# Performance work log

Hardware: AMD Instinct MI355X
Metric: run time of the kernel (lower is better)

## Reference

```python
import jax, jax.numpy as jnp
import numpy as np

N = 20000      # atoms
E = 320000     # edges
F = 128        # node_size (hard-pinned by split(128) / expand to 384)
RBF = 20
RC = 5.0
ITERS = 3
NM = 64        # molecules in batch


def setup_inputs() -> dict:
    key = jax.random.key(0)
    ks = iter(jax.random.split(key, 64))
    def nrm(shape, scale=0.05):
        return jax.random.normal(next(ks), shape, dtype=jnp.float32) * scale
    inp = {}
    inp["z"] = jax.random.randint(next(ks), (N,), 0, 119)
    inp["graph"] = jax.random.randint(next(ks), (E, 2), 0, N)
    inp["edges_dist"] = jax.random.uniform(next(ks), (E,), minval=0.5, maxval=RC, dtype=jnp.float32)
    sense = jax.random.normal(next(ks), (E, 3), dtype=jnp.float32)
    inp["edges_sense"] = sense / jnp.linalg.norm(sense, axis=1, keepdims=True)
    inp["graph_idx"] = jnp.sort(jax.random.randint(next(ks), (N,), 0, NM))
    # parameters (stacked over ITERS message/update blocks)
    inp["emb"] = nrm((119, F), 1.0)
    inp["mw1"] = nrm((ITERS, F, F)); inp["mb1"] = nrm((ITERS, F))
    inp["mw2"] = nrm((ITERS, 3 * F, F)); inp["mb2"] = nrm((ITERS, 3 * F))
    inp["ew"] = nrm((ITERS, 3 * F, RBF)); inp["eb"] = nrm((ITERS, 3 * F))
    inp["uw"] = nrm((ITERS, F, F)); inp["vw"] = nrm((ITERS, F, F))
    inp["aw1"] = nrm((ITERS, F, 2 * F)); inp["ab1"] = nrm((ITERS, F))
    inp["aw2"] = nrm((ITERS, 3 * F, F)); inp["ab2"] = nrm((ITERS, 3 * F))
    inp["ow1"] = nrm((F, F)); inp["ob1"] = nrm((F,))
    inp["ow2"] = nrm((1, F)); inp["ob2"] = nrm((1,))
    return inp


def reference(z, graph, edges_dist, edges_sense, graph_idx,
              emb, mw1, mb1, mw2, mb2, ew, eb,
              uw, vw, aw1, ab1, aw2, ab2, ow1, ob1, ow2, ob2):
    src = graph[:, 0]   # scatter target (index_add index)
    dst = graph[:, 1]   # gather source (neighbour)
    s = emb[z]                                  # [N, F]
    v = jnp.zeros((N, 3, F), dtype=s.dtype)     # [N, 3, F]
    # edge-level precompute (same every iteration)
    n = jnp.arange(1, RBF + 1, dtype=jnp.float32)
    d = edges_dist[:, None]
    rbf = jnp.sin(n * jnp.pi * d / RC) / d                              # [E, RBF]
    cut = 0.5 * (jnp.cos(jnp.pi * edges_dist / RC) + 1.0) * (edges_dist < RC)  # [E]
    for i in range(ITERS):
        # --- Message block ---
        a = jax.nn.silu(s @ mw1[i].T + mb1[i]) @ mw2[i].T + mb2[i]      # [N, 3F]
        dist_rep = (rbf @ ew[i].T + eb[i]) * cut[:, None]               # [E, 3F]
        res = a[dst] * dist_rep                                         # [E, 3F]
        rv, rs, rd = res[:, :F], res[:, F:2 * F], res[:, 2 * F:]
        resv = v[dst] * rv[:, None, :] + edges_sense[:, :, None] * rd[:, None, :]  # [E,3,F]
        s = s + 2.0 * jax.ops.segment_sum(rs, src, num_segments=N)
        v = v + 2.0 * jax.ops.segment_sum(resv, src, num_segments=N)
        # --- Update block ---
        Uv = v @ uw[i].T                                                # [N,3,F]
        Vv = v @ vw[i].T
        h = jnp.concatenate([s, jnp.linalg.norm(Vv, axis=1)], axis=-1)  # [N, 2F]
        a2 = jax.nn.silu(h @ aw1[i].T + ab1[i]) @ aw2[i].T + ab2[i]     # [N, 3F]
        avv, asv, ass = a2[:, :F], a2[:, F:2 * F], a2[:, 2 * F:]
        s = s + ass + asv * jnp.sum(Uv * Vv, axis=1)
        v = v + avv[:, None, :] * Uv
    out = jax.nn.silu(s @ ow1.T + ob1) @ ow2.T + ob2                    # [N, 1]
    return jax.ops.segment_sum(out, graph_idx, num_segments=NM)         # [NM, 1]
```

## Files before the change

kernel.cpp:

```cpp
#include <hip/hip_runtime.h>
#include <math.h>

#define NN 20000
#define NE 320000
#define FD 128
#define RBFN 20
#define RC_ 5.0f
#define NITER 3
#define NMOL 64
#define F3 384
#define F2 256
#define PI_ 3.14159265358979323846f
#define KB 128
#define LPAD 8
#define SDS 392

typedef __attribute__((ext_vector_type(8))) short  bf16x8;
typedef __attribute__((ext_vector_type(4))) float  floatx4;
typedef unsigned short u16;
typedef unsigned int   u32;

__device__ __forceinline__ u16 f2b(float x) {
    union { float f; unsigned int u; } v; v.f = x;
    unsigned int u = v.u;
    return (u16)((u + 0x7fffu + ((u >> 16) & 1u)) >> 16);
}
__device__ __forceinline__ float b2f(u16 x) {
    union { unsigned int u; float f; } v; v.u = ((unsigned int)x) << 16;
    return v.f;
}
__device__ __forceinline__ float blo(u32 w) {
    union { unsigned int u; float f; } v; v.u = w << 16; return v.f;
}
__device__ __forceinline__ float bhi(u32 w) {
    union { unsigned int u; float f; } v; v.u = w & 0xffff0000u; return v.f;
}
__device__ __forceinline__ u32 pack2(float a, float b) {
    return (u32)f2b(a) | ((u32)f2b(b) << 16);
}

__global__ __launch_bounds__(256) void init_all_kernel(
    const float* s0, int n0, const float* s1, int n1, const float* s2, int n2,
    const float* s3, int n3, const float* s4, int n4, const float* s5, int n5,
    const float* s6, int n6, u16* __restrict__ wdst,
    const float* __restrict__ ew, u16* __restrict__ ewb,
    const int* __restrict__ z, const float* __restrict__ emb,
    float* __restrict__ s, u16* __restrict__ sbf,
    float* __restrict__ v_a, int* __restrict__ v_pk_i, int* __restrict__ cnt)
{
    int idx = blockIdx.x * 256 + threadIdx.x;
    if (idx < NN * F3) v_a[idx] = 0.f;
    if (idx < NN * F3 / 2) v_pk_i[idx] = 0;
    if (idx < NN) cnt[idx] = 0;
    if (idx < NN * FD) {
        int n = idx >> 7, f = idx & 127;
        float v = emb[z[n] * FD + f];
        s[idx] = v; sbf[idx] = f2b(v);
    }
    if (idx < NITER * F3 * 32) {
        int k = idx & 31;
        int row = idx >> 5;
        ewb[idx] = (k < RBFN) ? f2b(ew[row * RBFN + k]) : (u16)0;
    }
    {
        int w = idx;
        u16* dst = wdst;
        if (w < n0) { dst[w] = f2b(s0[w]); return; } w -= n0; dst += n0;
        if (w < n1) { dst[w] = f2b(s1[w]); return; } w -= n1; dst += n1;
        if (w < n2) { dst[w] = f2b(s2[w]); return; } w -= n2; dst += n2;
        if (w < n3) { dst[w] = f2b(s3[w]); return; } w -= n3; dst += n3;
        if (w < n4) { dst[w] = f2b(s4[w]); return; } w -= n4; dst += n4;
        if (w < n5) { dst[w] = f2b(s5[w]); return; } w -= n5; dst += n5;
        if (w < n6) { dst[w] = f2b(s6[w]); }
    }
}

__global__ __launch_bounds__(256) void csr_count_kernel(const int* __restrict__ graph,
    int* __restrict__ cnt)
{
    int e = blockIdx.x * 256 + threadIdx.x;
    if (e >= NE) return;
    atomicAdd(&cnt[graph[2 * e]], 1);
}

__global__ __launch_bounds__(1024) void csr_scan_kernel(const int* __restrict__ cnt,
    int* __restrict__ row_ptr, int* __restrict__ cursor)
{
    __shared__ int sd[1024];
    int tid = threadIdx.x;
    const int chunk = (NN + 1023) / 1024;
    int start = tid * chunk;
    int end = start + chunk; if (end > NN) end = NN;
    int sum = 0;
    for (int j = start; j < end; j++) sum += cnt[j];
    sd[tid] = sum;
    __syncthreads();
    for (int off = 1; off < 1024; off <<= 1) {
        int v = 0;
        if (tid >= off) v = sd[tid - off];
        __syncthreads();
        if (tid >= off) sd[tid] += v;
        __syncthreads();
    }
    int run = (tid == 0) ? 0 : sd[tid - 1];
    for (int j = start; j < end; j++) {
        row_ptr[j] = run;
        cursor[j]  = run;
        run += cnt[j];
    }
    if (tid == 0) row_ptr[NN] = NE;
}

__global__ __launch_bounds__(256) void csr_scatter_kernel(const int* __restrict__ graph,
    int* __restrict__ cursor, int* __restrict__ edge_list)
{
    int e = blockIdx.x * 256 + threadIdx.x;
    if (e >= NE) return;
    int p = atomicAdd(&cursor[graph[2 * e]], 1);
    edge_list[p] = e;
}

__global__ __launch_bounds__(256) void edge_stream_kernel(
    const int* __restrict__ edge_list, const int* __restrict__ graph,
    const float* __restrict__ dist, const float* __restrict__ sense,
    u16* __restrict__ rbf_bf, float* __restrict__ cut_p,
    float* __restrict__ sense_p, int* __restrict__ dst_p)
{
    int j = blockIdx.x * 256 + threadIdx.x;
    if (j >= NE) return;
    int e = edge_list[j];
    float d = dist[e];
    float inv = 1.f / d;
    float base = PI_ * d / RC_;
    float s1, c1;
    __sincosf(base, &s1, &c1);
    float twoc = c1 + c1;
    u16* rb = rbf_bf + (size_t)j * 32;
    float sprev = 0.f, scur = s1;
    #pragma unroll
    for (int k = 0; k < RBFN; k++) {
        rb[k] = f2b(scur * inv);
        float snext = twoc * scur - sprev;
        sprev = scur; scur = snext;
    }
    #pragma unroll
    for (int k = RBFN; k < 32; k++) rb[k] = 0;
    cut_p[j] = 0.5f * (c1 + 1.f) * (d < RC_ ? 1.f : 0.f);
    dst_p[j] = graph[2 * e + 1];
    sense_p[3 * j + 0] = sense[3 * e + 0];
    sense_p[3 * j + 1] = sense[3 * e + 1];
    sense_p[3 * j + 2] = sense[3 * e + 2];
}

template<int K1, bool PACK>
__global__ __launch_bounds__(256) void mlp_kernel(const u16* __restrict__ A,
    const u16* __restrict__ W1, const float* __restrict__ b1,
    const u16* __restrict__ W2, const float* __restrict__ b2,
    u16* __restrict__ Ob, int M)
{
    __shared__ u16 As[64][KB + LPAD];
    __shared__ u16 Ws[128][KB + LPAD];
    __shared__ u16 T[64][KB + LPAD];
    const int bm = blockIdx.x * 64;
    const int tid = threadIdx.x;
    const int wave = tid >> 6, lane = tid & 63;
    const int wm  = (wave >> 1) * 32;
    const int wn1 = (wave & 1) * 64;
    const int wn  = (wave & 1) * 32;
    const int quad = lane >> 4, lr = lane & 15;
    const int r = tid >> 2, q = tid & 3;

    floatx4 acc1[2][4];
    #pragma unroll
    for (int i = 0; i < 2; i++)
        #pragma unroll
        for (int j = 0; j < 4; j++) acc1[i][j] = (floatx4)0.f;

    for (int ko = 0; ko < K1; ko += KB) {
        {
            int gm = bm + r;
            u16* dA = &As[r][q * 32];
            if (gm < M) {
                const u16* ap = A + (size_t)gm * K1 + ko + q * 32;
                #pragma unroll
                for (int x = 0; x < 32; x += 8)
                    *(bf16x8*)&dA[x] = *(const bf16x8*)(ap + x);
            } else {
                #pragma unroll
                for (int x = 0; x < 32; x += 8)
                    *(bf16x8*)&dA[x] = (bf16x8)0;
            }
            #pragma unroll
            for (int h = 0; h < 2; h++) {
                int wr = r + h * 64;
                const u16* wp = W1 + (size_t)wr * K1 + ko + q * 32;
                u16* dW = &Ws[wr][q * 32];
                #pragma unroll
                for (int x = 0; x < 32; x += 8)
                    *(bf16x8*)&dW[x] = *(const bf16x8*)(wp + x);
            }
        }
        __syncthreads();
        #pragma unroll
        for (int kk = 0; kk < KB; kk += 32) {
            bf16x8 a0 = *(const bf16x8*)&As[wm + lr     ][kk + quad * 8];
            bf16x8 a1 = *(const bf16x8*)&As[wm + 16 + lr][kk + quad * 8];
            #pragma unroll
            for (int j = 0; j < 4; j++) {
                bf16x8 b = *(const bf16x8*)&Ws[wn1 + j * 16 + lr][kk + quad * 8];
                acc1[0][j] = __builtin_amdgcn_mfma_f32_16x16x32_bf16(a0, b, acc1[0][j], 0, 0, 0);
                acc1[1][j] = __builtin_amdgcn_mfma_f32_16x16x32_bf16(a1, b, acc1[1][j], 0, 0, 0);
            }
        }
        __syncthreads();
    }
    #pragma unroll
    for (int i = 0; i < 2; i++) {
        #pragma unroll
        for (int j = 0; j < 4; j++) {
            int col = wn1 + j * 16 + lr;
            float bb = b1[col];
            #pragma unroll
            for (int rr = 0; rr < 4; rr++) {
                int row = wm + i * 16 + quad * 4 + rr;
                float v = acc1[i][j][rr] + bb;
                v = v / (1.f + __expf(-v));
                T[row][col] = f2b(v);
            }
        }
    }
    __syncthreads();

    for (int c0 = 0; c0 < F3; c0 += 64) {
        {
            const u16* wp = W2 + (size_t)(c0 + r) * KB + q * 32;
            u16* dW = &Ws[r][q * 32];
            #pragma unroll
            for (int x = 0; x < 32; x += 8)
                *(bf16x8*)&dW[x] = *(const bf16x8*)(wp + x);
        }
        __syncthreads();
        floatx4 acc2[2][2];
        #pragma unroll
        for (int i = 0; i < 2; i++)
            #pragma unroll
            for (int j = 0; j < 2; j++) acc2[i][j] = (floatx4)0.f;
        #pragma unroll
        for (int kk = 0; kk < KB; kk += 32) {
            bf16x8 a0 = *(const bf16x8*)&T[wm + lr     ][kk + quad * 8];
            bf16x8 a1 = *(const bf16x8*)&T[wm + 16 + lr][kk + quad * 8];
            bf16x8 b0 = *(const bf16x8*)&Ws[wn + lr     ][kk + quad * 8];
            bf16x8 b1 = *(const bf16x8*)&Ws[wn + 16 + lr][kk + quad * 8];
            acc2[0][0] = __builtin_amdgcn_mfma_f32_16x16x32_bf16(a0, b0, acc2[0][0], 0, 0, 0);
            acc2[0][1] = __builtin_amdgcn_mfma_f32_16x16x32_bf16(a0, b1, acc2[0][1], 0, 0, 0);
            acc2[1][0] = __builtin_amdgcn_mfma_f32_16x16x32_bf16(a1, b0, acc2[1][0], 0, 0, 0);
            acc2[1][1] = __builtin_amdgcn_mfma_f32_16x16x32_bf16(a1, b1, acc2[1][1], 0, 0, 0);
        }
        #pragma unroll
        for (int i = 0; i < 2; i++) {
            #pragma unroll
            for (int j = 0; j < 2; j++) {
                int gn = c0 + wn + j * 16 + lr;
                float bb = b2[gn];
                #pragma unroll
                for (int rr = 0; rr < 4; rr++) {
                    int gm = bm + wm + i * 16 + quad * 4 + rr;
                    if (gm < M) {
                        u16 val = f2b(acc2[i][j][rr] + bb);
                        if (PACK) {
                            int off = (gn < 256) ? ((gn & 127) * 2 + (gn >> 7))
                                                 : (256 + (gn & 127));
                            Ob[(size_t)gm * F3 + off] = val;
                        } else {
                            Ob[(size_t)gm * F3 + gn] = val;
                        }
                    }
                }
            }
        }
        __syncthreads();
    }
}

__global__ __launch_bounds__(256) void gemm_uv(const u16* __restrict__ A,
    const u16* __restrict__ Wu, const u16* __restrict__ Wv,
    u16* __restrict__ U, u16* __restrict__ V, int M)
{
    __shared__ u16 As[64][KB + LPAD];
    __shared__ u16 Bu[64][KB + LPAD];
    __shared__ u16 Bv[64][KB + LPAD];
    const int bm = blockIdx.x * 64;
    const int bn = blockIdx.y * 64;
    const int tid = threadIdx.x;
    const int r = tid >> 2;
    const int q = tid & 3;
    const int wave = tid >> 6;
    const int lane = tid & 63;
    const int wm = (wave >> 1) * 32;
    const int wn = (wave & 1) * 32;
    const int quad = lane >> 4;
    const int lr = lane & 15;

    floatx4 au[2][2], av[2][2];
    #pragma unroll
    for (int i = 0; i < 2; i++)
        #pragma unroll
        for (int j = 0; j < 2; j++) { au[i][j] = (floatx4)0.f; av[i][j] = (floatx4)0.f; }

    {
        int gm = bm + r;
        u16* dA = &As[r][q * 32];
        if (gm < M) {
            const u16* ap = A + (size_t)gm * KB + q * 32;
            #pragma unroll
            for (int x = 0; x < 32; x += 8)
                *(bf16x8*)&dA[x] = *(const bf16x8*)(ap + x);
        } else {
            #pragma unroll
            for (int x = 0; x < 32; x += 8)
                *(bf16x8*)&dA[x] = (bf16x8)0;
        }
        int gn = bn + r;
        const u16* up = Wu + (size_t)gn * KB + q * 32;
        const u16* vp = Wv + (size_t)gn * KB + q * 32;
        u16* dU = &Bu[r][q * 32];
        u16* dV = &Bv[r][q * 32];
        #pragma unroll
        for (int x = 0; x < 32; x += 8) {
            *(bf16x8*)&dU[x] = *(const bf16x8*)(up + x);
            *(bf16x8*)&dV[x] = *(const bf16x8*)(vp + x);
        }
    }
    __syncthreads();
    #pragma unroll
    for (int kk = 0; kk < KB; kk += 32) {
        bf16x8 a0 = *(const bf16x8*)&As[wm + lr     ][kk + quad * 8];
        bf16x8 a1 = *(const bf16x8*)&As[wm + 16 + lr][kk + quad * 8];
        bf16x8 u0 = *(const bf16x8*)&Bu[wn + lr     ][kk + quad * 8];
        bf16x8 u1 = *(const bf16x8*)&Bu[wn + 16 + lr][kk + quad * 8];
        bf16x8 v0 = *(const bf16x8*)&Bv[wn + lr     ][kk + quad * 8];
        bf16x8 v1 = *(const bf16x8*)&Bv[wn + 16 + lr][kk + quad * 8];
        au[0][0] = __builtin_amdgcn_mfma_f32_16x16x32_bf16(a0, u0, au[0][0], 0, 0, 0);
        au[0][1] = __builtin_amdgcn_mfma_f32_16x16x32_bf16(a0, u1, au[0][1], 0, 0, 0);
        au[1][0] = __builtin_amdgcn_mfma_f32_16x16x32_bf16(a1, u0, au[1][0], 0, 0, 0);
        au[1][1] = __builtin_amdgcn_mfma_f32_16x16x32_bf16(a1, u1, au[1][1], 0, 0, 0);
        av[0][0] = __builtin_amdgcn_mfma_f32_16x16x32_bf16(a0, v0, av[0][0], 0, 0, 0);
        av[0][1] = __builtin_amdgcn_mfma_f32_16x16x32_bf16(a0, v1, av[0][1], 0, 0, 0);
        av[1][0] = __builtin_amdgcn_mfma_f32_16x16x32_bf16(a1, v0, av[1][0], 0, 0, 0);
        av[1][1] = __builtin_amdgcn_mfma_f32_16x16x32_bf16(a1, v1, av[1][1], 0, 0, 0);
    }
    #pragma unroll
    for (int i = 0; i < 2; i++) {
        #pragma unroll
        for (int j = 0; j < 2; j++) {
            int gn = bn + wn + j * 16 + lr;
            #pragma unroll
            for (int rr = 0; rr < 4; rr++) {
                int gm = bm + wm + i * 16 + quad * 4 + rr;
                if (gm < M) {
                    U[(size_t)gm * FD + gn] = f2b(au[i][j][rr]);
                    V[(size_t)gm * FD + gn] = f2b(av[i][j][rr]);
                }
            }
        }
    }
}

__global__ __launch_bounds__(256) void edge_mfma_kernel(
    const u16* __restrict__ rbf_bf, const float* __restrict__ cut_p,
    const float* __restrict__ sense_p, const int* __restrict__ dst_p,
    const u16* __restrict__ ewb, const float* __restrict__ eb,
    const u16* __restrict__ a_pk, const float* __restrict__ s_in,
    const float* __restrict__ v_in, const u16* __restrict__ v_pk,
    const int* __restrict__ row_ptr,
    float* __restrict__ s_out, u16* __restrict__ s_obf,
    float* __restrict__ v_out, u16* __restrict__ v_obf)
{
    __shared__ u16   sdrep[16 * SDS];
    __shared__ float scut[16];
    __shared__ float ssen[16][4];
    __shared__ int   sdst[16];
    __shared__ float red[4 * 128];

    const int n = blockIdx.x;
    const int tid = threadIdx.x;
    const int wave = tid >> 6;
    const int lane = tid & 63;
    const int quad = lane >> 4;
    const int lr = lane & 15;
    const int f = tid & 127;
    const int half = tid >> 7;

    int beg = row_ptr[n], end = row_ptr[n + 1];
    float accs = 0.f, accv0 = 0.f, accv1 = 0.f, accv2 = 0.f;

    for (int t0 = beg; t0 < end; t0 += 16) {
        int cnt = end - t0; if (cnt > 16) cnt = 16;
        __syncthreads();
        if (tid < 16) {
            scut[tid] = (tid < cnt) ? cut_p[t0 + tid] : 0.f;
            sdst[tid] = (tid < cnt) ? dst_p[t0 + tid] : 0;
        }
        if (tid >= 64 && tid < 64 + 3 * cnt) {
            int x = tid - 64;
            ssen[x / 3][x % 3] = sense_p[3 * t0 + x];
        }
        bf16x8 afrag;
        int ge = t0 + lr;
        if (ge < end) afrag = *(const bf16x8*)&rbf_bf[(size_t)ge * 32 + quad * 8];
        else          afrag = (bf16x8)0;
        floatx4 dacc[6];
        #pragma unroll
        for (int nt = 0; nt < 6; nt++) {
            int nrow = (wave * 6 + nt) * 16 + lr;
            bf16x8 bfrag = *(const bf16x8*)&ewb[(size_t)nrow * 32 + quad * 8];
            dacc[nt] = __builtin_amdgcn_mfma_f32_16x16x32_bf16(afrag, bfrag, (floatx4)0.f, 0, 0, 0);
        }
        __syncthreads();
        #pragma unroll
        for (int nt = 0; nt < 6; nt++) {
            int ncol = (wave * 6 + nt) * 16 + lr;
            float ebn = eb[ncol];
            #pragma unroll
            for (int rr = 0; rr < 4; rr++) {
                int e = quad * 4 + rr;
                sdrep[e * SDS + ncol] = f2b((dacc[nt][rr] + ebn) * scut[e]);
            }
        }
        __syncthreads();
        int nh = cnt - half * 8; if (nh > 8) nh = 8;
        for (int k = 0; k < nh; k++) {
            int e = half * 8 + k;
            int dst = sdst[e];
            const u16* sr = &sdrep[e * SDS];
            float drv = b2f(sr[f]);
            float drs = b2f(sr[FD + f]);
            float drd = b2f(sr[2 * FD + f]);
            const u16* ar = a_pk + (size_t)dst * F3;
            u32 ap = *(const u32*)(ar + f * 2);
            float rv = b2f((u16)(ap & 0xffff)) * drv;
            float rs = b2f((u16)(ap >> 16))    * drs;
            float rd = b2f(ar[256 + f])        * drd;
            accs += rs;
            const u16* vr = v_pk + (size_t)dst * F3;
            u32 vp = *(const u32*)(vr + f * 2);
            accv0 += b2f((u16)(vp & 0xffff)) * rv + ssen[e][0] * rd;
            accv1 += b2f((u16)(vp >> 16))    * rv + ssen[e][1] * rd;
            accv2 += b2f(vr[256 + f])        * rv + ssen[e][2] * rd;
        }
    }
    __syncthreads();
    if (half == 1) {
        red[f] = accs; red[128 + f] = accv0; red[256 + f] = accv1; red[384 + f] = accv2;
    }
    __syncthreads();
    if (half == 0) {
        accs  += red[f];       accv0 += red[128 + f];
        accv1 += red[256 + f]; accv2 += red[384 + f];
        int nb = n * FD + f;
        float so = s_in[nb] + 2.f * accs;
        s_out[nb] = so; s_obf[nb] = f2b(so);
        int vb = n * F3 + f;
        float w0 = v_in[vb]           + 2.f * accv0;
        float w1 = v_in[vb + FD]      + 2.f * accv1;
        float w2 = v_in[vb + 2 * FD]  + 2.f * accv2;
        v_out[vb]          = w0; v_obf[vb]          = f2b(w0);
        v_out[vb + FD]     = w1; v_obf[vb + FD]     = f2b(w1);
        v_out[vb + 2 * FD] = w2; v_obf[vb + 2 * FD] = f2b(w2);
    }
}

template<bool LAST>
__global__ __launch_bounds__(256) void mlp2_update_next_kernel(
    const u16* __restrict__ sbf_mid, const float* __restrict__ s_mid,
    const float* __restrict__ v_mid,
    const u16* __restrict__ Uv, const u16* __restrict__ Vv,
    const u16* __restrict__ W1, const float* __restrict__ b1,
    const u16* __restrict__ W2, const float* __restrict__ b2,
    float* __restrict__ s_out,
    float* __restrict__ v_out, u16* __restrict__ v_pk,
    const u16* __restrict__ N_W1, const float* __restrict__ N_b1,
    const u16* __restrict__ N_W2, const float* __restrict__ N_b2,
    u16* __restrict__ a_pk,
    const u16* __restrict__ H_W1, const float* __restrict__ H_b1,
    const float* __restrict__ ow2, const float* __restrict__ ob2,
    float* __restrict__ nodeval, int M)
{
    __shared__ u16 As[64][KB + LPAD];
    __shared__ u16 Ws[128][KB + LPAD];
    __shared__ u16 T[64][KB + LPAD];
    const int bm = blockIdx.x * 64;
    const int tid = threadIdx.x;
    const int wave = tid >> 6, lane = tid & 63;
    const int wm  = (wave >> 1) * 32;
    const int wn1 = (wave & 1) * 64;
    const int wn  = (wave & 1) * 32;
    const int quad = lane >> 4, lr = lane & 15;
    const int r = tid >> 2, q = tid & 3;

    floatx4 acc1[2][4];
    #pragma unroll
    for (int i = 0; i < 2; i++)
        #pragma unroll
        for (int j = 0; j < 4; j++) acc1[i][j] = (floatx4)0.f;

    {
        int gm = bm + r;
        u16* dA = &As[r][q * 32];
        if (gm < M) {
            const u16* ap = sbf_mid + (size_t)gm * FD + q * 32;
            #pragma unroll
            for (int x = 0; x < 32; x += 8)
                *(bf16x8*)&dA[x] = *(const bf16x8*)(ap + x);
        } else {
            #pragma unroll
            for (int x = 0; x < 32; x += 8)
                *(bf16x8*)&dA[x] = (bf16x8)0;
        }
        #pragma unroll
        for (int h = 0; h < 2; h++) {
            int wr = r + h * 64;
            const u16* wp = W1 + (size_t)wr * F2 + q * 32;
            u16* dW = &Ws[wr][q * 32];
            #pragma unroll
            for (int x = 0; x < 32; x += 8)
                *(bf16x8*)&dW[x] = *(const bf16x8*)(wp + x);
        }
    }
    __syncthreads();
    #pragma unroll
    for (int kk = 0; kk < KB; kk += 32) {
        bf16x8 a0 = *(const bf16x8*)&As[wm + lr     ][kk + quad * 8];
        bf16x8 a1 = *(const bf16x8*)&As[wm + 16 + lr][kk + quad * 8];
        #pragma unroll
        for (int j = 0; j < 4; j++) {
            bf16x8 b = *(const bf16x8*)&Ws[wn1 + j * 16 + lr][kk + quad * 8];
            acc1[0][j] = __builtin_amdgcn_mfma_f32_16x16x32_bf16(a0, b, acc1[0][j], 0, 0, 0);
            acc1[1][j] = __builtin_amdgcn_mfma_f32_16x16x32_bf16(a1, b, acc1[1][j], 0, 0, 0);
        }
    }
    __syncthreads();
    {
        int gm = bm + r;
        u16* dA = &As[r][q * 32];
        if (gm < M) {
            const u16* vvp = Vv + (size_t)gm * F3 + q * 32;
            bf16x8 c0[4], c1[4], c2[4];
            #pragma unroll
            for (int t = 0; t < 4; t++) {
                c0[t] = *(const bf16x8*)(vvp + t * 8);
                c1[t] = *(const bf16x8*)(vvp + FD + t * 8);
                c2[t] = *(const bf16x8*)(vvp + 2 * FD + t * 8);
            }
            #pragma unroll
            for (int t = 0; t < 4; t++) {
                #pragma unroll
                for (int x = 0; x < 8; x++) {
                    float a = b2f((u16)c0[t][x]);
                    float b = b2f((u16)c1[t][x]);
                    float c = b2f((u16)c2[t][x]);
                    dA[t * 8 + x] = f2b(sqrtf(a * a + b * b + c * c));
                }
            }
        } else {
            #pragma unroll
            for (int x = 0; x < 32; x += 8)
                *(bf16x8*)&dA[x] = (bf16x8)0;
        }
        #pragma unroll
        for (int h = 0; h < 2; h++) {
            int wr = r + h * 64;
            const u16* wp = W1 + (size_t)wr * F2 + KB + q * 32;
            u16* dW = &Ws[wr][q * 32];
            #pragma unroll
            for (int x = 0; x < 32; x += 8)
                *(bf16x8*)&dW[x] = *(const bf16x8*)(wp + x);
        }
    }
    __syncthreads();
    #pragma unroll
    for (int kk = 0; kk < KB; kk += 32) {
        bf16x8 a0 = *(const bf16x8*)&As[wm + lr     ][kk + quad * 8];
        bf16x8 a1 = *(const bf16x8*)&As[wm + 16 + lr][kk + quad * 8];
        #pragma unroll
        for (int j = 0; j < 4; j++) {
            bf16x8 b = *(const bf16x8*)&Ws[wn1 + j * 16 + lr][kk + quad * 8];
            acc1[0][j] = __builtin_amdgcn_mfma_f32_16x16x32_bf16(a0, b, acc1[0][j], 0, 0, 0);
            acc1[1][j] = __builtin_amdgcn_mfma_f32_16x16x32_bf16(a1, b, acc1[1][j], 0, 0, 0);
        }
    }
    __syncthreads();
    #pragma unroll
    for (int i = 0; i < 2; i++) {
        #pragma unroll
        for (int j = 0; j < 4; j++) {
            int col = wn1 + j * 16 + lr;
            float bb = b1[col];
            #pragma unroll
            for (int rr = 0; rr < 4; rr++) {
                int row = wm + i * 16 + quad * 4 + rr;
                float v = acc1[i][j][rr] + bb;
                v = v / (1.f + __expf(-v));
                T[row][col] = f2b(v);
            }
        }
    }
    __syncthreads();

    float avvr[2][2][4], asvr[2][2][4];
    #pragma unroll
    for (int part = 0; part < 2; part++) {
        #pragma unroll
        for (int piece = 0; piece < 3; piece++) {
            const int c0 = piece * 128 + part * 64;
            {
                const u16* wp = W2 + (size_t)(c0 + r) * KB + q * 32;
                u16* dW = &Ws[r][q * 32];
                #pragma unroll
                for (int x = 0; x < 32; x += 8)
                    *(bf16x8*)&dW[x] = *(const bf16x8*)(wp + x);
            }
            __syncthreads();
            floatx4 acc2[2][2];
            #pragma unroll
            for (int i = 0; i < 2; i++)
                #pragma unroll
                for (int j = 0; j < 2; j++) acc2[i][j] = (floatx4)0.f;
            #pragma unroll
            for (int kk = 0; kk < KB; kk += 32) {
                bf16x8 a0 = *(const bf16x8*)&T[wm + lr     ][kk + quad * 8];
                bf16x8 a1 = *(const bf16x8*)&T[wm + 16 + lr][kk + quad * 8];
                bf16x8 b0 = *(const bf16x8*)&Ws[wn + lr     ][kk + quad * 8];
                bf16x8 b1 = *(const bf16x8*)&Ws[wn + 16 + lr][kk + quad * 8];
                acc2[0][0] = __builtin_amdgcn_mfma_f32_16x16x32_bf16(a0, b0, acc2[0][0], 0, 0, 0);
                acc2[0][1] = __builtin_amdgcn_mfma_f32_16x16x32_bf16(a0, b1, acc2[0][1], 0, 0, 0);
                acc2[1][0] = __builtin_amdgcn_mfma_f32_16x16x32_bf16(a1, b0, acc2[1][0], 0, 0, 0);
                acc2[1][1] = __builtin_amdgcn_mfma_f32_16x16x32_bf16(a1, b1, acc2[1][1], 0, 0, 0);
            }
            if (piece == 0) {
                #pragma unroll
                for (int i = 0; i < 2; i++)
                    #pragma unroll
                    for (int j = 0; j < 2; j++) {
                        int gn = c0 + wn + j * 16 + lr;
                        float bb = b2[gn];
                        #pragma unroll
                        for (int rr = 0; rr < 4; rr++)
                            avvr[i][j][rr] = acc2[i][j][rr] + bb;
                    }
            } else if (piece == 1) {
                #pragma unroll
                for (int i = 0; i < 2; i++)
                    #pragma unroll
                    for (int j = 0; j < 2; j++) {
                        int gn = c0 + wn + j * 16 + lr;
                        float bb = b2[gn];
                        #pragma unroll
                        for (int rr = 0; rr < 4; rr++)
                            asvr[i][j][rr] = acc2[i][j][rr] + bb;
                    }
            } else {
                #pragma unroll
                for (int i = 0; i < 2; i++) {
                    #pragma unroll
                    for (int j = 0; j < 2; j++) {
                        int gn = c0 + wn + j * 16 + lr;
                        int f  = gn - 256;
                        float bb = b2[gn];
                        #pragma unroll
                        for (int rr = 0; rr < 4; rr++) {
                            int row = wm + i * 16 + quad * 4 + rr;
                            int gm = bm + row;
                            if (gm < M) {
                                float ass = acc2[i][j][rr] + bb;
                                float asv = asvr[i][j][rr];
                                float avv = avvr[i][j][rr];
                                int vb = gm * F3 + f;
                                float u0 = b2f(Uv[vb]);
                                float u1 = b2f(Uv[vb + FD]);
                                float u2 = b2f(Uv[vb + 2 * FD]);
                                float w0 = b2f(Vv[vb]);
                                float w1 = b2f(Vv[vb + FD]);
                                float w2 = b2f(Vv[vb + 2 * FD]);
                                float dot = u0 * w0 + u1 * w1 + u2 * w2;
                                int nb = gm * FD + f;
                                float so = s_mid[nb] + ass + asv * dot;
                                s_out[nb] = so;
                                As[row][f] = f2b(so);
                                float y0 = v_mid[vb]          + avv * u0;
                                float y1 = v_mid[vb + FD]     + avv * u1;
                                float y2 = v_mid[vb + 2 * FD] + avv * u2;
                                v_out[vb]          = y0;
                                v_out[vb + FD]     = y1;
                                v_out[vb + 2 * FD] = y2;
                                char* vpb = (char*)v_pk + (size_t)gm * (2 * F3);
                                *(u32*)(vpb + 4 * f) = pack2(y0, y1);
                                *(u16*)(vpb + 512 + 2 * f) = f2b(y2);
                            } else {
                                As[row][f] = 0;
                            }
                        }
                    }
                }
            }
            __syncthreads();
        }
    }

    if constexpr (!LAST) {
        {
            #pragma unroll
            for (int h = 0; h < 2; h++) {
                int wr = r + h * 64;
                const u16* wp = N_W1 + (size_t)wr * KB + q * 32;
                u16* dW = &Ws[wr][q * 32];
                #pragma unroll
                for (int x = 0; x < 32; x += 8)
                    *(bf16x8*)&dW[x] = *(const bf16x8*)(wp + x);
            }
        }
        __syncthreads();
        #pragma unroll
        for (int i = 0; i < 2; i++)
            #pragma unroll
            for (int j = 0; j < 4; j++) acc1[i][j] = (floatx4)0.f;
        #pragma unroll
        for (int kk = 0; kk < KB; kk += 32) {
            bf16x8 a0 = *(const bf16x8*)&As[wm + lr     ][kk + quad * 8];
            bf16x8 a1 = *(const bf16x8*)&As[wm + 16 + lr][kk + quad * 8];
            #pragma unroll
            for (int j = 0; j < 4; j++) {
                bf16x8 b = *(const bf16x8*)&Ws[wn1 + j * 16 + lr][kk + quad * 8];
                acc1[0][j] = __builtin_amdgcn_mfma_f32_16x16x32_bf16(a0, b, acc1[0][j], 0, 0, 0);
                acc1[1][j] = __builtin_amdgcn_mfma_f32_16x16x32_bf16(a1, b, acc1[1][j], 0, 0, 0);
            }
        }
        __syncthreads();
        #pragma unroll
        for (int i = 0; i < 2; i++) {
            #pragma unroll
            for (int j = 0; j < 4; j++) {
                int col = wn1 + j * 16 + lr;
                float bb = N_b1[col];
                #pragma unroll
                for (int rr = 0; rr < 4; rr++) {
                    int row = wm + i * 16 + quad * 4 + rr;
                    float v = acc1[i][j][rr] + bb;
                    v = v / (1.f + __expf(-v));
                    T[row][col] = f2b(v);
                }
            }
        }
        __syncthreads();
        for (int c0 = 0; c0 < F3; c0 += 64) {
            {
                const u16* wp = N_W2 + (size_t)(c0 + r) * KB + q * 32;
                u16* dW = &Ws[r][q * 32];
                #pragma unroll
                for (int x = 0; x < 32; x += 8)
                    *(bf16x8*)&dW[x] = *(const bf16x8*)(wp + x);
            }
            __syncthreads();
            floatx4 acc2[2][2];
            #pragma unroll
            for (int i = 0; i < 2; i++)
                #pragma unroll
                for (int j = 0; j < 2; j++) acc2[i][j] = (floatx4)0.f;
            #pragma unroll
            for (int kk = 0; kk < KB; kk += 32) {
                bf16x8 a0 = *(const bf16x8*)&T[wm + lr     ][kk + quad * 8];
                bf16x8 a1 = *(const bf16x8*)&T[wm + 16 + lr][kk + quad * 8];
                bf16x8 b0 = *(const bf16x8*)&Ws[wn + lr     ][kk + quad * 8];
                bf16x8 b1 = *(const bf16x8*)&Ws[wn + 16 + lr][kk + quad * 8];
                acc2[0][0] = __builtin_amdgcn_mfma_f32_16x16x32_bf16(a0, b0, acc2[0][0], 0, 0, 0);
                acc2[0][1] = __builtin_amdgcn_mfma_f32_16x16x32_bf16(a0, b1, acc2[0][1], 0, 0, 0);
                acc2[1][0] = __builtin_amdgcn_mfma_f32_16x16x32_bf16(a1, b0, acc2[1][0], 0, 0, 0);
                acc2[1][1] = __builtin_amdgcn_mfma_f32_16x16x32_bf16(a1, b1, acc2[1][1], 0, 0, 0);
            }
            #pragma unroll
            for (int i = 0; i < 2; i++) {
                #pragma unroll
                for (int j = 0; j < 2; j++) {
                    int gn = c0 + wn + j * 16 + lr;
                    float bb = N_b2[gn];
                    #pragma unroll
                    for (int rr = 0; rr < 4; rr++) {
                        int gm = bm + wm + i * 16 + quad * 4 + rr;
                        if (gm < M) {
                            u16 val = f2b(acc2[i][j][rr] + bb);
                            int off = (gn < 256) ? ((gn & 127) * 2 + (gn >> 7))
                                                 : (256 + (gn & 127));
                            a_pk[(size_t)gm * F3 + off] = val;
                        }
                    }
                }
            }
            __syncthreads();
        }
    } else {
        {
            #pragma unroll
            for (int h = 0; h < 2; h++) {
                int wr = r + h * 64;
                const u16* wp = H_W1 + (size_t)wr * KB + q * 32;
                u16* dW = &Ws[wr][q * 32];
                #pragma unroll
                for (int x = 0; x < 32; x += 8)
                    *(bf16x8*)&dW[x] = *(const bf16x8*)(wp + x);
            }
        }
        __syncthreads();
        #pragma unroll
        for (int i = 0; i < 2; i++)
            #pragma unroll
            for (int j = 0; j < 4; j++) acc1[i][j] = (floatx4)0.f;
        #pragma unroll
        for (int kk = 0; kk < KB; kk += 32) {
            bf16x8 a0 = *(const bf16x8*)&As[wm + lr     ][kk + quad * 8];
            bf16x8 a1 = *(const bf16x8*)&As[wm + 16 + lr][kk + quad * 8];
            #pragma unroll
            for (int j = 0; j < 4; j++) {
                bf16x8 b = *(const bf16x8*)&Ws[wn1 + j * 16 + lr][kk + quad * 8];
                acc1[0][j] = __builtin_amdgcn_mfma_f32_16x16x32_bf16(a0, b, acc1[0][j], 0, 0, 0);
                acc1[1][j] = __builtin_amdgcn_mfma_f32_16x16x32_bf16(a1, b, acc1[1][j], 0, 0, 0);
            }
        }
        __syncthreads();
        float* Tf   = (float*)&Ws[0][0];
        float* ow2s = (float*)&As[0][0];
        if (tid < KB) ow2s[tid] = ow2[tid];
        #pragma unroll
        for (int i = 0; i < 2; i++) {
            #pragma unroll
            for (int j = 0; j < 4; j++) {
                int col = wn1 + j * 16 + lr;
                float bb = H_b1[col];
                #pragma unroll
                for (int rr = 0; rr < 4; rr++) {
                    int row = wm + i * 16 + quad * 4 + rr;
                    float v = acc1[i][j][rr] + bb;
                    v = v / (1.f + __expf(-v));
                    Tf[row * 132 + col] = v;
                }
            }
        }
        __syncthreads();
        int nl = tid >> 2, seg = tid & 3;
        float v = 0.f;
        #pragma unroll
        for (int x = 0; x < 32; x++) {
            int col = seg * 32 + x;
            v += Tf[nl * 132 + col] * ow2s[col];
        }
        v += __shfl_down(v, 2);
        v += __shfl_down(v, 1);
        if (seg == 0) {
            int gm = bm + nl;
            if (gm < M) nodeval[gm] = v + ob2[0];
        }
    }
}

__global__ __launch_bounds__(1024) void mol_reduce_kernel(const float* __restrict__ nodeval,
    const int* __restrict__ gidx, float* __restrict__ out)
{
    __shared__ float mol[NMOL];
    int tid = threadIdx.x;
    if (tid < NMOL) mol[tid] = 0.f;
    __syncthreads();
    int cur = -1; float acc = 0.f;
    for (int x = tid; x < NN; x += 1024) {
        int g = gidx[x];
        float v = nodeval[x];
        if (g != cur) {
            if (cur >= 0) atomicAdd(&mol[cur], acc);
            cur = g; acc = v;
        } else acc += v;
    }
    if (cur >= 0) atomicAdd(&mol[cur], acc);
    __syncthreads();
    if (tid < NMOL) out[tid] = mol[tid];
}

extern "C" void kernel_launch(void* const* d_in, const int* in_sizes, int n_in,
                              void* d_out, int out_size, void* d_ws, size_t ws_size,
                              hipStream_t stream)
{
    const int*   z     = (const int*)d_in[0];
    const int*   graph = (const int*)d_in[1];
    const float* dist  = (const float*)d_in[2];
    const float* sense = (const float*)d_in[3];
    const int*   gidx  = (const int*)d_in[4];
    const float* emb   = (const float*)d_in[5];
    const float* mw1   = (const float*)d_in[6];
    const float* mb1   = (const float*)d_in[7];
    const float* mw2   = (const float*)d_in[8];
    const float* mb2   = (const float*)d_in[9];
    const float* ew    = (const float*)d_in[10];
    const float* eb    = (const float*)d_in[11];
    const float* uw    = (const float*)d_in[12];
    const float* vw    = (const float*)d_in[13];
    const float* aw1   = (const float*)d_in[14];
    const float* ab1   = (const float*)d_in[15];
    const float* aw2   = (const float*)d_in[16];
    const float* ab2   = (const float*)d_in[17];
    const float* ow1   = (const float*)d_in[18];
    const float* ob1   = (const float*)d_in[19];
    const float* ow2   = (const float*)d_in[20];
    const float* ob2   = (const float*)d_in[21];
    float* out = (float*)d_out;

    float* W = (float*)d_ws;
    float* s_a    = W; W += (size_t)NN * FD;
    float* s_b    = W; W += (size_t)NN * FD;
    float* v_a    = W; W += (size_t)NN * F3;
    float* v_b    = W; W += (size_t)NN * F3;
    float* cut_p  = W; W += (size_t)NE;
    float* sns_p  = W; W += (size_t)NE * 3;
    float* nodeval= W; W += (size_t)NN;
    u16* U = (u16*)W;
    u16* sbf_a = U; U += (size_t)NN * FD;
    u16* sbf_b = U; U += (size_t)NN * FD;
    u16* vbf_b = U; U += (size_t)NN * F3;
    u16* a_pk  = U; U += (size_t)NN * F3;
    u16* v_pk  = U; U += (size_t)NN * F3;
    u16* h_bf  = U; U += (size_t)NN * F2;
    u16* a2_bf = U; U += (size_t)NN * F3;
    u16* Uv_bf = U; U += (size_t)NN * F3;
    u16* Vv_bf = U; U += (size_t)NN * F3;
    u16* rbf_bf= U; U += (size_t)NE * 32;
    u16* ewb   = U; U += (size_t)NITER * F3 * 32;
    u16* wb    = U; U += 557056;
    int* ip = (int*)U;
    int* row_ptr   = ip; ip += NN + 1;
    int* cnt       = ip; ip += NN;
    int* cursor    = ip; ip += NN;
    int* edge_list = ip; ip += NE;
    int* dst_p     = ip; ip += NE;

    u16* wb_mw1 = wb;
    u16* wb_mw2 = wb + 49152;
    u16* wb_uw  = wb + 196608;
    u16* wb_vw  = wb + 245760;
    u16* wb_aw1 = wb + 294912;
    u16* wb_aw2 = wb + 393216;
    u16* wb_ow1 = wb + 540672;

    const int TB = 256;
    dim3 b256(TB);

    init_all_kernel<<<dim3((NN * F3 + TB - 1) / TB), b256, 0, stream>>>(
        mw1, 49152, mw2, 147456, uw, 49152, vw, 49152, aw1, 98304, aw2, 147456,
        ow1, 16384, wb, ew, ewb, z, emb, s_a, sbf_a, v_a, (int*)v_pk, cnt);
    csr_count_kernel<<<dim3((NE + TB - 1) / TB), b256, 0, stream>>>(graph, cnt);
    csr_scan_kernel<<<dim3(1), dim3(1024), 0, stream>>>(cnt, row_ptr, cursor);
    csr_scatter_kernel<<<dim3((NE + TB - 1) / TB), b256, 0, stream>>>(graph, cursor, edge_list);
    edge_stream_kernel<<<dim3((NE + TB - 1) / TB), b256, 0, stream>>>(
        edge_list, graph, dist, sense, rbf_bf, cut_p, sns_p, dst_p);

    dim3 gM((NN + 63) / 64);
    dim3 gV2((3 * NN + 63) / 64, FD / 64);

    mlp_kernel<128, true><<<gM, b256, 0, stream>>>(sbf_a,
        wb_mw1, mb1, wb_mw2, mb2, a_pk, NN);

    for (int i = 0; i < NITER; i++) {
        edge_mfma_kernel<<<dim3(NN), b256, 0, stream>>>(
            rbf_bf, cut_p, sns_p, dst_p,
            ewb + (size_t)i * F3 * 32, eb + (size_t)i * F3,
            a_pk, s_a, v_a, v_pk, row_ptr, s_b, sbf_b, v_b, vbf_b);
        gemm_uv<<<gV2, b256, 0, stream>>>(vbf_b, wb_uw + (size_t)i * FD * FD,
            wb_vw + (size_t)i * FD * FD, Uv_bf, Vv_bf, 3 * NN);
        if (i < NITER - 1) {
            mlp2_update_next_kernel<false><<<gM, b256, 0, stream>>>(
                sbf_b, s_b, v_b, Uv_bf, Vv_bf,
                wb_aw1 + (size_t)i * FD * F2, ab1 + (size_t)i * FD,
                wb_aw2 + (size_t)i * F3 * FD, ab2 + (size_t)i * F3,
                s_a, v_a, v_pk,
                wb_mw1 + (size_t)(i + 1) * FD * FD, mb1 + (size_t)(i + 1) * FD,
                wb_mw2 + (size_t)(i + 1) * F3 * FD, mb2 + (size_t)(i + 1) * F3, a_pk,
                nullptr, nullptr, nullptr, nullptr, nullptr, NN);
        } else {
            mlp2_update_next_kernel<true><<<gM, b256, 0, stream>>>(
                sbf_b, s_b, v_b, Uv_bf, Vv_bf,
                wb_aw1 + (size_t)i * FD * F2, ab1 + (size_t)i * FD,
                wb_aw2 + (size_t)i * F3 * FD, ab2 + (size_t)i * F3,
                s_a, v_a, v_pk,
                nullptr, nullptr, nullptr, nullptr, nullptr,
                wb_ow1, ob1, ow2, ob2, nodeval, NN);
        }
    }

    mol_reduce_kernel<<<dim3(1), dim3(1024), 0, stream>>>(nodeval, gidx, out);
}
```

Before: 868.5 us.

## Double-buffer W2 tiles in update MLP and merge gemm_uv column tiles

In the update/next-message kernel, the second-layer weight tiles are now double-buffered across two halves of the shared Ws buffer. Each 64-column slice is prefetched while the current one is multiplied, which removes one barrier per slice. gemm_uv now runs one block per 64-row tile and loops over both 64-column output tiles, so the A tile is loaded from global memory once instead of twice, at the cost of half as many blocks. This assumes Ws already has room for 128 rows; the diff does not change its declaration.

```diff
diff --git a/kernel.cpp b/kernel.cpp
--- a/kernel.cpp
+++ b/kernel.cpp
@@ -290,7 +290,6 @@
     __shared__ u16 Bu[64][KB + LPAD];
     __shared__ u16 Bv[64][KB + LPAD];
     const int bm = blockIdx.x * 64;
-    const int bn = blockIdx.y * 64;
     const int tid = threadIdx.x;
     const int r = tid >> 2;
     const int q = tid & 3;
@@ -301,12 +300,6 @@
     const int quad = lane >> 4;
     const int lr = lane & 15;
 
-    floatx4 au[2][2], av[2][2];
-    #pragma unroll
-    for (int i = 0; i < 2; i++)
-        #pragma unroll
-        for (int j = 0; j < 2; j++) { au[i][j] = (floatx4)0.f; av[i][j] = (floatx4)0.f; }
-
     {
         int gm = bm + r;
         u16* dA = &As[r][q * 32];
@@ -320,49 +313,61 @@
             for (int x = 0; x < 32; x += 8)
                 *(bf16x8*)&dA[x] = (bf16x8)0;
         }
-        int gn = bn + r;
-        const u16* up = Wu + (size_t)gn * KB + q * 32;
-        const u16* vp = Wv + (size_t)gn * KB + q * 32;
-        u16* dU = &Bu[r][q * 32];
-        u16* dV = &Bv[r][q * 32];
-        #pragma unroll
-        for (int x = 0; x < 32; x += 8) {
-            *(bf16x8*)&dU[x] = *(const bf16x8*)(up + x);
-            *(bf16x8*)&dV[x] = *(const bf16x8*)(vp + x);
-        }
-    }
-    __syncthreads();
+    }
+
     #pragma unroll
-    for (int kk = 0; kk < KB; kk += 32) {
-        bf16x8 a0 = *(const bf16x8*)&As[wm + lr     ][kk + quad * 8];
-        bf16x8 a1 = *(const bf16x8*)&As[wm + 16 + lr][kk + quad * 8];
-        bf16x8 u0 = *(const bf16x8*)&Bu[wn + lr     ][kk + quad * 8];
-        bf16x8 u1 = *(const bf16x8*)&Bu[wn + 16 + lr][kk + quad * 8];
-        bf16x8 v0 = *(const bf16x8*)&Bv[wn + lr     ][kk + quad * 8];
-        bf16x8 v1 = *(const bf16x8*)&Bv[wn + 16 + lr][kk + quad * 8];
-        au[0][0] = __builtin_amdgcn_mfma_f32_16x16x32_bf16(a0, u0, au[0][0], 0, 0, 0);
-        au[0][1] = __builtin_amdgcn_mfma_f32_16x16x32_bf16(a0, u1, au[0][1], 0, 0, 0);
-        au[1][0] = __builtin_amdgcn_mfma_f32_16x16x32_bf16(a1, u0, au[1][0], 0, 0, 0);
-        au[1][1] = __builtin_amdgcn_mfma_f32_16x16x32_bf16(a1, u1, au[1][1], 0, 0, 0);
-        av[0][0] = __builtin_amdgcn_mfma_f32_16x16x32_bf16(a0, v0, av[0][0], 0, 0, 0);
-        av[0][1] = __builtin_amdgcn_mfma_f32_16x16x32_bf16(a0, v1, av[0][1], 0, 0, 0);
-        av[1][0] = __builtin_amdgcn_mfma_f32_16x16x32_bf16(a1, v0, av[1][0], 0, 0, 0);
-        av[1][1] = __builtin_amdgcn_mfma_f32_16x16x32_bf16(a1, v1, av[1][1], 0, 0, 0);
-    }
-    #pragma unroll
-    for (int i = 0; i < 2; i++) {
-        #pragma unroll
-        for (int j = 0; j < 2; j++) {
-            int gn = bn + wn + j * 16 + lr;
-            #pragma unroll
-            for (int rr = 0; rr < 4; rr++) {
-                int gm = bm + wm + i * 16 + quad * 4 + rr;
-                if (gm < M) {
-                    U[(size_t)gm * FD + gn] = f2b(au[i][j][rr]);
-                    V[(size_t)gm * FD + gn] = f2b(av[i][j][rr]);
+    for (int bn = 0; bn < FD; bn += 64) {
+        {
+            int gn = bn + r;
+            const u16* up = Wu + (size_t)gn * KB + q * 32;
+            const u16* vp = Wv + (size_t)gn * KB + q * 32;
+            u16* dU = &Bu[r][q * 32];
+            u16* dV = &Bv[r][q * 32];
+            #pragma unroll
+            for (int x = 0; x < 32; x += 8) {
+                *(bf16x8*)&dU[x] = *(const bf16x8*)(up + x);
+                *(bf16x8*)&dV[x] = *(const bf16x8*)(vp + x);
+            }
+        }
+        __syncthreads();
+        floatx4 au[2][2], av[2][2];
+        #pragma unroll
+        for (int i = 0; i < 2; i++)
+            #pragma unroll
+            for (int j = 0; j < 2; j++) { au[i][j] = (floatx4)0.f; av[i][j] = (floatx4)0.f; }
+        #pragma unroll
+        for (int kk = 0; kk < KB; kk += 32) {
+            bf16x8 a0 = *(const bf16x8*)&As[wm + lr     ][kk + quad * 8];
+            bf16x8 a1 = *(const bf16x8*)&As[wm + 16 + lr][kk + quad * 8];
+            bf16x8 u0 = *(const bf16x8*)&Bu[wn + lr     ][kk + quad * 8];
+            bf16x8 u1 = *(const bf16x8*)&Bu[wn + 16 + lr][kk + quad * 8];
+            bf16x8 v0 = *(const bf16x8*)&Bv[wn + lr     ][kk + quad * 8];
+            bf16x8 v1 = *(const bf16x8*)&Bv[wn + 16 + lr][kk + quad * 8];
+            au[0][0] = __builtin_amdgcn_mfma_f32_16x16x32_bf16(a0, u0, au[0][0], 0, 0, 0);
+            au[0][1] = __builtin_amdgcn_mfma_f32_16x16x32_bf16(a0, u1, au[0][1], 0, 0, 0);
+            au[1][0] = __builtin_amdgcn_mfma_f32_16x16x32_bf16(a1, u0, au[1][0], 0, 0, 0);
+            au[1][1] = __builtin_amdgcn_mfma_f32_16x16x32_bf16(a1, u1, au[1][1], 0, 0, 0);
+            av[0][0] = __builtin_amdgcn_mfma_f32_16x16x32_bf16(a0, v0, av[0][0], 0, 0, 0);
+            av[0][1] = __builtin_amdgcn_mfma_f32_16x16x32_bf16(a0, v1, av[0][1], 0, 0, 0);
+            av[1][0] = __builtin_amdgcn_mfma_f32_16x16x32_bf16(a1, v0, av[1][0], 0, 0, 0);
+            av[1][1] = __builtin_amdgcn_mfma_f32_16x16x32_bf16(a1, v1, av[1][1], 0, 0, 0);
+        }
+        #pragma unroll
+        for (int i = 0; i < 2; i++) {
+            #pragma unroll
+            for (int j = 0; j < 2; j++) {
+                int gn = bn + wn + j * 16 + lr;
+                #pragma unroll
+                for (int rr = 0; rr < 4; rr++) {
+                    int gm = bm + wm + i * 16 + quad * 4 + rr;
+                    if (gm < M) {
+                        U[(size_t)gm * FD + gn] = f2b(au[i][j][rr]);
+                        V[(size_t)gm * FD + gn] = f2b(av[i][j][rr]);
+                    }
                 }
             }
         }
+        __syncthreads();
     }
 }
 
@@ -605,106 +610,114 @@
             }
         }
     }
+
+    float avvr[2][2][4], asvr[2][2][4];
+    {
+        const u16* wp = W2 + (size_t)r * KB + q * 32;
+        u16* dW = &Ws[r][q * 32];
+        #pragma unroll
+        for (int x = 0; x < 32; x += 8)
+            *(bf16x8*)&dW[x] = *(const bf16x8*)(wp + x);
+    }
     __syncthreads();
-
-    float avvr[2][2][4], asvr[2][2][4];
     #pragma unroll
-    for (int part = 0; part < 2; part++) {
-        #pragma unroll
-        for (int piece = 0; piece < 3; piece++) {
-            const int c0 = piece * 128 + part * 64;
-            {
-                const u16* wp = W2 + (size_t)(c0 + r) * KB + q * 32;
-                u16* dW = &Ws[r][q * 32];
-                #pragma unroll
-                for (int x = 0; x < 32; x += 8)
-                    *(bf16x8*)&dW[x] = *(const bf16x8*)(wp + x);
-            }
-            __syncthreads();
-            floatx4 acc2[2][2];
+    for (int pp = 0; pp < 6; pp++) {
+        const int part  = pp / 3;
+        const int piece = pp % 3;
+        const int c0 = piece * 128 + part * 64;
+        const int hcur = (pp & 1) * 64;
+        if (pp < 5) {
+            const int c0n = ((pp + 1) % 3) * 128 + ((pp + 1) / 3) * 64;
+            const int hnext = ((pp + 1) & 1) * 64;
+            const u16* wp = W2 + (size_t)(c0n + r) * KB + q * 32;
+            u16* dW = &Ws[hnext + r][q * 32];
+            #pragma unroll
+            for (int x = 0; x < 32; x += 8)
+                *(bf16x8*)&dW[x] = *(const bf16x8*)(wp + x);
+        }
+        floatx4 acc2[2][2];
+        #pragma unroll
+        for (int i = 0; i < 2; i++)
+            #pragma unroll
+            for (int j = 0; j < 2; j++) acc2[i][j] = (floatx4)0.f;
+        #pragma unroll
+        for (int kk = 0; kk < KB; kk += 32) {
+            bf16x8 a0 = *(const bf16x8*)&T[wm + lr     ][kk + quad * 8];
+            bf16x8 a1 = *(const bf16x8*)&T[wm + 16 + lr][kk + quad * 8];
+            bf16x8 b0 = *(const bf16x8*)&Ws[hcur + wn + lr     ][kk + quad * 8];
+            bf16x8 b1 = *(const bf16x8*)&Ws[hcur + wn + 16 + lr][kk + quad * 8];
+            acc2[0][0] = __builtin_amdgcn_mfma_f32_16x16x32_bf16(a0, b0, acc2[0][0], 0, 0, 0);
+            acc2[0][1] = __builtin_amdgcn_mfma_f32_16x16x32_bf16(a0, b1, acc2[0][1], 0, 0, 0);
+            acc2[1][0] = __builtin_amdgcn_mfma_f32_16x16x32_bf16(a1, b0, acc2[1][0], 0, 0, 0);
+            acc2[1][1] = __builtin_amdgcn_mfma_f32_16x16x32_bf16(a1, b1, acc2[1][1], 0, 0, 0);
+        }
+        if (piece == 0) {
             #pragma unroll
             for (int i = 0; i < 2; i++)
                 #pragma unroll
-                for (int j = 0; j < 2; j++) acc2[i][j] = (floatx4)0.f;
-            #pragma unroll
-            for (int kk = 0; kk < KB; kk += 32) {
-                bf16x8 a0 = *(const bf16x8*)&T[wm + lr     ][kk + quad * 8];
-                bf16x8 a1 = *(const bf16x8*)&T[wm + 16 + lr][kk + quad * 8];
-                bf16x8 b0 = *(const bf16x8*)&Ws[wn + lr     ][kk + quad * 8];
-                bf16x8 b1 = *(const bf16x8*)&Ws[wn + 16 + lr][kk + quad * 8];
-                acc2[0][0] = __builtin_amdgcn_mfma_f32_16x16x32_bf16(a0, b0, acc2[0][0], 0, 0, 0);
-                acc2[0][1] = __builtin_amdgcn_mfma_f32_16x16x32_bf16(a0, b1, acc2[0][1], 0, 0, 0);
-                acc2[1][0] = __builtin_amdgcn_mfma_f32_16x16x32_bf16(a1, b0, acc2[1][0], 0, 0, 0);
-                acc2[1][1] = __builtin_amdgcn_mfma_f32_16x16x32_bf16(a1, b1, acc2[1][1], 0, 0, 0);
-            }
-            if (piece == 0) {
-                #pragma unroll
-                for (int i = 0; i < 2; i++)
+                for (int j = 0; j < 2; j++) {
+                    int gn = c0 + wn + j * 16 + lr;
+                    float bb = b2[gn];
                     #pragma unroll
-                    for (int j = 0; j < 2; j++) {
-                        int gn = c0 + wn + j * 16 + lr;
-                        float bb = b2[gn];
-                        #pragma unroll
-                        for (int rr = 0; rr < 4; rr++)
-                            avvr[i][j][rr] = acc2[i][j][rr] + bb;
-                    }
-            } else if (piece == 1) {
-                #pragma unroll
-                for (int i = 0; i < 2; i++)
+                    for (int rr = 0; rr < 4; rr++)
+                        avvr[i][j][rr] = acc2[i][j][rr] + bb;
+                }
+        } else if (piece == 1) {
+            #pragma unroll
+            for (int i = 0; i < 2; i++)
+                #pragma unroll
+                for (int j = 0; j < 2; j++) {
+                    int gn = c0 + wn + j * 16 + lr;
+                    float bb = b2[gn];
                     #pragma unroll
-                    for (int j = 0; j < 2; j++) {
-                        int gn = c0 + wn + j * 16 + lr;
-                        float bb = b2[gn];
-                        #pragma unroll
-                        for (int rr = 0; rr < 4; rr++)
-                            asvr[i][j][rr] = acc2[i][j][rr] + bb;
-                    }
-            } else {
-                #pragma unroll
-                for (int i = 0; i < 2; i++) {
+                    for (int rr = 0; rr < 4; rr++)
+                        asvr[i][j][rr] = acc2[i][j][rr] + bb;
+                }
+        } else {
+            #pragma unroll
+            for (int i = 0; i < 2; i++) {
+                #pragma unroll
+                for (int j = 0; j < 2; j++) {
+                    int gn = c0 + wn + j * 16 + lr;
+                    int f  = gn - 256;
+                    float bb = b2[gn];
                     #pragma unroll
-                    for (int j = 0; j < 2; j++) {
-                        int gn = c0 + wn + j * 16 + lr;
-                        int f  = gn - 256;
-                        float bb = b2[gn];
-                        #pragma unroll
-                        for (int rr = 0; rr < 4; rr++) {
-                            int row = wm + i * 16 + quad * 4 + rr;
-                            int gm = bm + row;
-                            if (gm < M) {
-                                float ass = acc2[i][j][rr] + bb;
-                                float asv = asvr[i][j][rr];
-                                float avv = avvr[i][j][rr];
-                                int vb = gm * F3 + f;
-                                float u0 = b2f(Uv[vb]);
-                                float u1 = b2f(Uv[vb + FD]);
-                                float u2 = b2f(Uv[vb + 2 * FD]);
-                                float w0 = b2f(Vv[vb]);
-                                float w1 = b2f(Vv[vb + FD]);
-                                float w2 = b2f(Vv[vb + 2 * FD]);
-                                float dot = u0 * w0 + u1 * w1 + u2 * w2;
-                                int nb = gm * FD + f;
-                                float so = s_mid[nb] + ass + asv * dot;
-                                s_out[nb] = so;
-                                As[row][f] = f2b(so);
-                                float y0 = v_mid[vb]          + avv * u0;
-                                float y1 = v_mid[vb + FD]     + avv * u1;
-                                float y2 = v_mid[vb + 2 * FD] + avv * u2;
-                                v_out[vb]          = y0;
-                                v_out[vb + FD]     = y1;
-                                v_out[vb + 2 * FD] = y2;
-                                char* vpb = (char*)v_pk + (size_t)gm * (2 * F3);
-                                *(u32*)(vpb + 4 * f) = pack2(y0, y1);
-                                *(u16*)(vpb + 512 + 2 * f) = f2b(y2);
-                            } else {
-                                As[row][f] = 0;
-                            }
+                    for (int rr = 0; rr < 4; rr++) {
+                        int row = wm + i * 16 + quad * 4 + rr;
+                        int gm = bm + row;
+                        if (gm < M) {
+                            float ass = acc2[i][j][rr] + bb;
+                            float asv = asvr[i][j][rr];
+                            float avv = avvr[i][j][rr];
+                            int vb = gm * F3 + f;
+                            float u0 = b2f(Uv[vb]);
+                            float u1 = b2f(Uv[vb + FD]);
+                            float u2 = b2f(Uv[vb + 2 * FD]);
+                            float w0 = b2f(Vv[vb]);
+                            float w1 = b2f(Vv[vb + FD]);
+                            float w2 = b2f(Vv[vb + 2 * FD]);
+                            float dot = u0 * w0 + u1 * w1 + u2 * w2;
+                            int nb = gm * FD + f;
+                            float so = s_mid[nb] + ass + asv * dot;
+                            s_out[nb] = so;
+                            As[row][f] = f2b(so);
+                            float y0 = v_mid[vb]          + avv * u0;
+                            float y1 = v_mid[vb + FD]     + avv * u1;
+                            float y2 = v_mid[vb + 2 * FD] + avv * u2;
+                            v_out[vb]          = y0;
+                            v_out[vb + FD]     = y1;
+                            v_out[vb + 2 * FD] = y2;
+                            char* vpb = (char*)v_pk + (size_t)gm * (2 * F3);
+                            *(u32*)(vpb + 4 * f) = pack2(y0, y1);
+                            *(u16*)(vpb + 512 + 2 * f) = f2b(y2);
+                        } else {
+                            As[row][f] = 0;
                         }
                     }
                 }
             }
-            __syncthreads();
-        }
+        }
+        __syncthreads();
     }
 
     if constexpr (!LAST) {
@@ -751,16 +764,26 @@
                 }
             }
         }
-        __syncthreads();
-        for (int c0 = 0; c0 < F3; c0 += 64) {
-            {
-                const u16* wp = N_W2 + (size_t)(c0 + r) * KB + q * 32;
-                u16* dW = &Ws[r][q * 32];
+        {
+            const u16* wp = N_W2 + (size_t)r * KB + q * 32;
+            u16* dW = &Ws[r][q * 32];
+            #pragma unroll
+            for (int x = 0; x < 32; x += 8)
+                *(bf16x8*)&dW[x] = *(const bf16x8*)(wp + x);
+        }
+        __syncthreads();
+        #pragma unroll
+        for (int pp = 0; pp < 6; pp++) {
+            const int c0 = pp * 64;
+            const int hcur = (pp & 1) * 64;
+            if (pp < 5) {
+                const int hnext = ((pp + 1) & 1) * 64;
+                const u16* wp = N_W2 + (size_t)((pp + 1) * 64 + r) * KB + q * 32;
+                u16* dW = &Ws[hnext + r][q * 32];
                 #pragma unroll
                 for (int x = 0; x < 32; x += 8)
                     *(bf16x8*)&dW[x] = *(const bf16x8*)(wp + x);
             }
-            __syncthreads();
             floatx4 acc2[2][2];
             #pragma unroll
             for (int i = 0; i < 2; i++)
@@ -770,8 +793,8 @@
             for (int kk = 0; kk < KB; kk += 32) {
                 bf16x8 a0 = *(const bf16x8*)&T[wm + lr     ][kk + quad * 8];
                 bf16x8 a1 = *(const bf16x8*)&T[wm + 16 + lr][kk + quad * 8];
-                bf16x8 b0 = *(const bf16x8*)&Ws[wn + lr     ][kk + quad * 8];
-                bf16x8 b1 = *(const bf16x8*)&Ws[wn + 16 + lr][kk + quad * 8];
+                bf16x8 b0 = *(const bf16x8*)&Ws[hcur + wn + lr     ][kk + quad * 8];
+                bf16x8 b1 = *(const bf16x8*)&Ws[hcur + wn + 16 + lr][kk + quad * 8];
                 acc2[0][0] = __builtin_amdgcn_mfma_f32_16x16x32_bf16(a0, b0, acc2[0][0], 0, 0, 0);
                 acc2[0][1] = __builtin_amdgcn_mfma_f32_16x16x32_bf16(a0, b1, acc2[0][1], 0, 0, 0);
                 acc2[1][0] = __builtin_amdgcn_mfma_f32_16x16x32_bf16(a1, b0, acc2[1][0], 0, 0, 0);
@@ -959,7 +982,7 @@
         edge_list, graph, dist, sense, rbf_bf, cut_p, sns_p, dst_p);
 
     dim3 gM((NN + 63) / 64);
-    dim3 gV2((3 * NN + 63) / 64, FD / 64);
+    dim3 gUV((3 * NN + 63) / 64);
 
     mlp_kernel<128, true><<<gM, b256, 0, stream>>>(sbf_a,
         wb_mw1, mb1, wb_mw2, mb2, a_pk, NN);
@@ -969,7 +992,7 @@
             rbf_bf, cut_p, sns_p, dst_p,
             ewb + (size_t)i * F3 * 32, eb + (size_t)i * F3,
             a_pk, s_a, v_a, v_pk, row_ptr, s_b, sbf_b, v_b, vbf_b);
-        gemm_uv<<<gV2, b256, 0, stream>>>(vbf_b, wb_uw + (size_t)i * FD * FD,
+        gemm_uv<<<gUV, b256, 0, stream>>>(vbf_b, wb_uw + (size_t)i * FD * FD,
             wb_vw + (size_t)i * FD * FD, Uv_bf, Vv_bf, 3 * NN);
         if (i < NITER - 1) {
             mlp2_update_next_kernel<false><<<gM, b256, 0, stream>>>(
```

Result: no change. 864.6 us (-0.4%).
